# Kernel tuning notes

Measured on AMD Instinct MI355X. Metric: run time of the kernel, lower is better.

## Reference

```python
import jax, jax.numpy as jnp
import numpy as np

EPS = 1e-12  # tf.nn.l2_normalize epsilon


def _l2norm(x, axis):
    # tf.nn.l2_normalize: x / sqrt(max(sum(x^2), eps))
    return x * jax.lax.rsqrt(jnp.maximum(jnp.sum(x * x, axis=axis, keepdims=True), EPS))


def setup_inputs() -> dict:
    key = jax.random.key(0)
    k0, k1, k2, k3 = jax.random.split(key, 4)
    B, L, E, C, NG = 128, 1024, 300, 20, 55
    return {
        "x_emb": jax.random.normal(k0, (B, L, E), jnp.float32),
        "x_mask": jnp.ones((B, L), jnp.float32),            # mask_seq = tf.ones(...) in call()
        "W_class": jax.random.normal(k1, (B, C, E), jnp.float32),
        "conv_w": jax.random.normal(k2, (NG, C, C), jnp.float32) * 0.05,  # [width, in=C, out=C]
        "conv_b": jnp.zeros((C,), jnp.float32),
        "W_dis": jax.random.normal(k3, (C, E), jnp.float32) * 0.05,       # 20 per-class 0-layer discriminators
        "b_dis": jnp.zeros((C,), jnp.float32),
    }


def reference(x_emb, x_mask, W_class, conv_w, conv_b, W_dis, b_dis):
    # --- att_emb_ngram_encoder_cnn ---
    x0 = x_emb * x_mask[..., None]                       # b s e (masked word embeddings)
    xn = _l2norm(x0, 2)                                  # b s e
    wn = _l2norm(W_class, 2)                             # b c e (normalize over embed dim)
    G = jnp.einsum('bse,bce->bsc', xn, wn)               # cosine label-word attention, b s c
    # ngram conv smoothing over sequence, SAME padding, relu
    att = jax.lax.conv_general_dilated(
        G, conv_w, window_strides=(1,), padding='SAME',
        dimension_numbers=('NWC', 'WIO', 'NWC')) + conv_b  # b s c
    att = jax.nn.relu(att)
    # partial (masked) softmax over sequence dim
    ew = jnp.exp(att) * x_mask[..., None]                # b s c
    beta = ew / jnp.sum(ew, axis=1, keepdims=True)       # b s c
    # per-class attentive pooling of (unmasked) word embeddings: H_enc b e c
    H = jnp.einsum('bse,bsc->bec', x_emb, beta)
    # --- 20 per-class 0-layer discriminators (dropout is identity at inference) ---
    logits = jnp.einsum('bec,ce->bc', H, W_dis) + b_dis  # b c
    return logits
```

## Files before the change

### kernel.cpp

```cpp
#include <hip/hip_runtime.h>
#include <math.h>

#define B 128
#define L 1024
#define E 300
#define C 20

#define OFF_WNT 0
#define OFF_WDT 768000
#define OFF_SWC 774000
#define OFF_G   796400
#define OFF_D   3417840
#define OFF_S   6039280
#define OFF_T   6041840

__global__ __launch_bounds__(256) void prep_kernel(
    const float* __restrict__ Wc, const float* __restrict__ convw,
    const float* __restrict__ wdis,
    float* __restrict__ wnT, float* __restrict__ wdT,
    float* __restrict__ swc, float* __restrict__ ST)
{
  int t = threadIdx.x;
  int gid = blockIdx.x * 256 + t;

  if (gid < 2 * B * C) ST[gid] = 0.f;

  if (gid < 55 * C * C) {
    int w  = gid / (C * C);
    int r  = gid % (C * C);
    int ci = r / C, co = r % C;
    swc[(((size_t)ci * 4 + co / 5) * 14 + (w >> 2)) * 20 + (co % 5) * 4 + (w & 3)] = convw[gid];
  }
  if (gid < C * C) {
    int ci = gid / C, co = gid % C;
    swc[(((size_t)ci * 4 + co / 5) * 14 + 13) * 20 + (co % 5) * 4 + 3] = 0.f;
  }
  if (gid < 6000) {
    int og = gid / 1500, rem = gid % 1500;
    int kq = rem / 20, i = rem % 20;
    int co = og * 5 + i / 4, q = i & 3;
    wdT[gid] = wdis[(size_t)co * E + kq * 4 + q];
  }

  int row = blockIdx.x * 4 + (t >> 6);
  int ln  = t & 63;
  if (row < B * C) {
    int bb = row / C, c = row % C;
    const float* src = Wc + (size_t)row * E;
    float v[5];
    float ss = 0.f;
    #pragma unroll
    for (int k = 0; k < 5; ++k) {
      int e = ln + 64 * k;
      v[k] = (e < E) ? src[e] : 0.f;
      ss += v[k] * v[k];
    }
    #pragma unroll
    for (int off = 32; off; off >>= 1) ss += __shfl_xor(ss, off, 64);
    float r = rsqrtf(fmaxf(ss, 1e-12f));
    float* dst = wnT + ((size_t)bb * 4 + c / 5) * 1500;
    int cosub = (c % 5) * 4;
    #pragma unroll
    for (int k = 0; k < 5; ++k) {
      int e = ln + 64 * k;
      if (e < E) dst[(e >> 2) * 20 + cosub + (e & 3)] = v[k] * r;
    }
  }
}

__global__ __launch_bounds__(512, 4) void gemm_kernel(
    const float* __restrict__ x, const float* __restrict__ wnT,
    const float* __restrict__ wdT, float* __restrict__ Gt, float* __restrict__ Dt)
{
  __shared__ float xs[32 * 256];

  int t  = threadIdx.x;
  int ln = t & 63;
  int wid  = __builtin_amdgcn_readfirstlane(t >> 6);
  int og   = wid & 3;
  int role = wid >> 2;
  int b  = blockIdx.y;
  int s0 = blockIdx.x * 256;

  const float* wbase = (role == 0) ? (wnT + ((size_t)b * 4 + og) * 1500)
                                   : (wdT + (size_t)og * 1500);

  float acc[5][4];
  #pragma unroll
  for (int c = 0; c < 5; ++c)
    #pragma unroll
    for (int j = 0; j < 4; ++j) acc[c][j] = 0.f;
  float ssq[4] = {0.f, 0.f, 0.f, 0.f};

  for (int chunk = 0; chunk < 10; ++chunk) {
    int k0 = chunk * 32;
    int krem = E - k0; if (krem > 32) krem = 32;

    const float* xb = x + ((size_t)b * L + s0) * E + k0;
    #pragma unroll
    for (int it = 0; it < 4; ++it) {
      int idx = it * 512 + t;
      int row = idx >> 3, col = idx & 7;
      if (col * 4 < krem) {
        float4 f = *(const float4*)(xb + (size_t)row * E + col * 4);
        xs[(col * 4 + 0) * 256 + row] = f.x;
        xs[(col * 4 + 1) * 256 + row] = f.y;
        xs[(col * 4 + 2) * 256 + row] = f.z;
        xs[(col * 4 + 3) * 256 + row] = f.w;
      }
    }
    __syncthreads();

    int nq = krem >> 2;
    #pragma unroll
    for (int kq = 0; kq < 8; ++kq) {
      if (kq < nq) {
        const float* wp = wbase + (chunk * 8 + kq) * 20;
        float w[20];
        #pragma unroll
        for (int i = 0; i < 20; ++i) w[i] = wp[i];
        float4 xk[4];
        #pragma unroll
        for (int q = 0; q < 4; ++q)
          xk[q] = *(const float4*)&xs[(kq * 4 + q) * 256 + ln * 4];
        if (wid == 0) {
          #pragma unroll
          for (int q = 0; q < 4; ++q) {
            const float* xf = (const float*)&xk[q];
            #pragma unroll
            for (int j = 0; j < 4; ++j) ssq[j] = fmaf(xf[j], xf[j], ssq[j]);
          }
        }
        #pragma unroll
        for (int q = 0; q < 4; ++q) {
          const float* xf = (const float*)&xk[q];
          #pragma unroll
          for (int c = 0; c < 5; ++c) {
            float wv = w[c * 4 + q];
            #pragma unroll
            for (int j = 0; j < 4; ++j) acc[c][j] = fmaf(xf[j], wv, acc[c][j]);
          }
        }
      }
    }
    __syncthreads();
  }

  if (wid == 0) {
    #pragma unroll
    for (int j = 0; j < 4; ++j) xs[ln * 4 + j] = rsqrtf(fmaxf(ssq[j], 1e-12f));
  }
  __syncthreads();

  int s = s0 + ln * 4;
  if (role == 0) {
    float4 rv = *(const float4*)&xs[ln * 4];
    const float* rf = (const float*)&rv;
    #pragma unroll
    for (int c = 0; c < 5; ++c) {
      float4 o = { acc[c][0] * rf[0], acc[c][1] * rf[1],
                   acc[c][2] * rf[2], acc[c][3] * rf[3] };
      *(float4*)&Gt[((size_t)b * C + og * 5 + c) * L + s] = o;
    }
  } else {
    #pragma unroll
    for (int c = 0; c < 5; ++c) {
      float4 o = { acc[c][0], acc[c][1], acc[c][2], acc[c][3] };
      *(float4*)&Dt[((size_t)b * C + og * 5 + c) * L + s] = o;
    }
  }
}

#define GP 312
__global__ __launch_bounds__(512, 4) void conv_kernel(
    const float* __restrict__ Gt, const float* __restrict__ Dt,
    const float* __restrict__ swc, const float* __restrict__ convb,
    float* __restrict__ S, float* __restrict__ T)
{
  __shared__ float g_lds[C * GP];

  int t  = threadIdx.x;
  int ln = t & 63;
  int wid = __builtin_amdgcn_readfirstlane(t >> 6);
  int og  = wid & 3;
  int cih = wid >> 2;
  int b  = blockIdx.y;
  int s0 = blockIdx.x * 256;

  for (int c = 0; c < C; ++c)
    for (int h = t; h < GP; h += 512) {
      int s = s0 - 27 + h;
      g_lds[c * GP + h] = (s >= 0 && s < L) ? Gt[((size_t)b * C + c) * L + s] : 0.f;
    }
  __syncthreads();

  float acc[4][5];
  #pragma unroll
  for (int j = 0; j < 4; ++j)
    #pragma unroll
    for (int c = 0; c < 5; ++c) acc[j][c] = 0.f;

  for (int ci = cih * 10; ci < cih * 10 + 10; ++ci) {
    const float* gl = &g_lds[ci * GP + ln * 4];
    const float* wp = swc + ((size_t)ci * 4 + og) * 280;
    float4 g0 = *(const float4*)gl;
    #pragma unroll
    for (int wq = 0; wq < 14; ++wq) {
      float4 g1 = *(const float4*)(gl + wq * 4 + 4);
      float w[20];
      #pragma unroll
      for (int i = 0; i < 20; ++i) w[i] = wp[wq * 20 + i];
      float ga[7] = {g0.x, g0.y, g0.z, g0.w, g1.x, g1.y, g1.z};
      #pragma unroll
      for (int q = 0; q < 4; ++q) {
        #pragma unroll
        for (int j = 0; j < 4; ++j) {
          float gv = ga[q + j];
          #pragma unroll
          for (int c = 0; c < 5; ++c)
            acc[j][c] = fmaf(gv, w[c * 4 + q], acc[j][c]);
        }
      }
      g0 = g1;
    }
  }

  __syncthreads();
  float* scr = g_lds;
  int pr = (og * 64 + ln) * 21;
  if (cih == 1) {
    #pragma unroll
    for (int j = 0; j < 4; ++j)
      #pragma unroll
      for (int c = 0; c < 5; ++c) scr[pr + j * 5 + c] = acc[j][c];
  }
  __syncthreads();

  if (cih == 0) {
    #pragma unroll
    for (int j = 0; j < 4; ++j)
      #pragma unroll
      for (int c = 0; c < 5; ++c) acc[j][c] += scr[pr + j * 5 + c];

    float se[5], st_[5];
    int s = s0 + ln * 4;
    #pragma unroll
    for (int c = 0; c < 5; ++c) {
      float cb = convb[og * 5 + c];
      float4 d4 = *(const float4*)&Dt[((size_t)b * C + og * 5 + c) * L + s];
      const float* df = (const float*)&d4;
      float e0 = 0.f, e1 = 0.f;
      #pragma unroll
      for (int j = 0; j < 4; ++j) {
        float a = acc[j][c] + cb;
        float e = expf(fmaxf(a, 0.f));
        e0 += e;
        e1 += e * df[j];
      }
      se[c] = e0; st_[c] = e1;
    }
    #pragma unroll
    for (int c = 0; c < 5; ++c) {
      #pragma unroll
      for (int off = 32; off; off >>= 1) {
        se[c]  += __shfl_xor(se[c],  off, 64);
        st_[c] += __shfl_xor(st_[c], off, 64);
      }
    }
    if (ln == 0) {
      #pragma unroll
      for (int c = 0; c < 5; ++c) {
        atomicAdd(&S[b * C + og * 5 + c], se[c]);
        atomicAdd(&T[b * C + og * 5 + c], st_[c]);
      }
    }
  }
}

__global__ __launch_bounds__(256) void fin_kernel(
    const float* __restrict__ S, const float* __restrict__ T,
    const float* __restrict__ bdis, float* __restrict__ out)
{
  int i = blockIdx.x * 256 + threadIdx.x;
  if (i < B * C) out[i] = T[i] / S[i] + bdis[i % C];
}

extern "C" void kernel_launch(void* const* d_in, const int* in_sizes, int n_in,
                              void* d_out, int out_size, void* d_ws, size_t ws_size,
                              hipStream_t stream) {
  const float* x_emb = (const float*)d_in[0];
  const float* Wc    = (const float*)d_in[2];
  const float* convw = (const float*)d_in[3];
  const float* convb = (const float*)d_in[4];
  const float* wdis  = (const float*)d_in[5];
  const float* bdis  = (const float*)d_in[6];

  float* ws  = (float*)d_ws;
  float* wnT = ws + OFF_WNT;
  float* wdT = ws + OFF_WDT;
  float* swc = ws + OFF_SWC;
  float* Gt  = ws + OFF_G;
  float* Dt  = ws + OFF_D;
  float* S   = ws + OFF_S;
  float* T   = ws + OFF_T;
  float* out = (float*)d_out;

  prep_kernel<<<640, 256, 0, stream>>>(Wc, convw, wdis, wnT, wdT, swc, S);
  gemm_kernel<<<dim3(L / 256, B), 512, 0, stream>>>(x_emb, wnT, wdT, Gt, Dt);
  conv_kernel<<<dim3(L / 256, B), 512, 0, stream>>>(Gt, Dt, swc, convb, S, T);
  fin_kernel<<<10, 256, 0, stream>>>(S, T, bdis, out);
}
```

Measured before the change: 330.7 us.

## Retile projection GEMM with row-major padded LDS, register prefetch, wider output groups

The GEMM kernel is retiled to 128-row blocks of 256 threads. Each wave now computes 10 output columns for 2 rows instead of 5 columns for 4 rows, so the weight layouts in prep are regrouped into halves of 10 classes. x is stored row-major in LDS with a padded stride of 33, which replaces the transposed scalar stores with float4 stores. The next chunk is prefetched into registers while the current one is computed. Conv kernel launch bounds are raised to 6 blocks per CU, which trades register budget for occupancy and risks spills.

Result: slower. 427.9 us (+29.4%).

```diff
diff --git a/kernel.cpp b/kernel.cpp
--- a/kernel.cpp
+++ b/kernel.cpp
@@ -36,10 +36,10 @@
     swc[(((size_t)ci * 4 + co / 5) * 14 + 13) * 20 + (co % 5) * 4 + 3] = 0.f;
   }
   if (gid < 6000) {
-    int og = gid / 1500, rem = gid % 1500;
-    int kq = rem / 20, i = rem % 20;
-    int co = og * 5 + i / 4, q = i & 3;
-    wdT[gid] = wdis[(size_t)co * E + kq * 4 + q];
+    int h = gid / 3000, rem = gid % 3000;
+    int kq = rem / 40, i = rem % 40;
+    int o = i >> 2, q = i & 3;
+    wdT[gid] = wdis[(size_t)(h * 10 + o) * E + kq * 4 + q];
   }
 
   int row = blockIdx.x * 4 + (t >> 6);
@@ -58,87 +58,100 @@
     #pragma unroll
     for (int off = 32; off; off >>= 1) ss += __shfl_xor(ss, off, 64);
     float r = rsqrtf(fmaxf(ss, 1e-12f));
-    float* dst = wnT + ((size_t)bb * 4 + c / 5) * 1500;
-    int cosub = (c % 5) * 4;
+    float* dst = wnT + ((size_t)bb * 2 + c / 10) * 3000;
+    int cosub = (c % 10) * 4;
     #pragma unroll
     for (int k = 0; k < 5; ++k) {
       int e = ln + 64 * k;
-      if (e < E) dst[(e >> 2) * 20 + cosub + (e & 3)] = v[k] * r;
-    }
-  }
-}
-
-__global__ __launch_bounds__(512, 4) void gemm_kernel(
+      if (e < E) dst[(e >> 2) * 40 + cosub + (e & 3)] = v[k] * r;
+    }
+  }
+}
+
+#define KSTR 33
+__global__ __launch_bounds__(256, 4) void gemm_kernel(
     const float* __restrict__ x, const float* __restrict__ wnT,
     const float* __restrict__ wdT, float* __restrict__ Gt, float* __restrict__ Dt)
 {
-  __shared__ float xs[32 * 256];
+  __shared__ float xs[128 * KSTR];
+  __shared__ float rinvS[128];
 
   int t  = threadIdx.x;
   int ln = t & 63;
   int wid  = __builtin_amdgcn_readfirstlane(t >> 6);
-  int og   = wid & 3;
-  int role = wid >> 2;
+  int h    = wid & 1;
+  int role = wid >> 1;
   int b  = blockIdx.y;
-  int s0 = blockIdx.x * 256;
-
-  const float* wbase = (role == 0) ? (wnT + ((size_t)b * 4 + og) * 1500)
-                                   : (wdT + (size_t)og * 1500);
-
-  float acc[5][4];
+  int s0 = blockIdx.x * 128;
+
+  const float* wbase = (role == 0) ? (wnT + ((size_t)b * 2 + h) * 3000)
+                                   : (wdT + (size_t)h * 3000);
+  const float* xb = x + ((size_t)b * L + s0) * E;
+
+  float acc[10][2];
   #pragma unroll
-  for (int c = 0; c < 5; ++c)
-    #pragma unroll
-    for (int j = 0; j < 4; ++j) acc[c][j] = 0.f;
-  float ssq[4] = {0.f, 0.f, 0.f, 0.f};
+  for (int o = 0; o < 10; ++o) { acc[o][0] = 0.f; acc[o][1] = 0.f; }
+  float ssq0 = 0.f, ssq1 = 0.f;
+
+  float4 pf[4];
+  #pragma unroll
+  for (int it = 0; it < 4; ++it) {
+    int idx = it * 256 + t;
+    int row = idx >> 3, col = idx & 7;
+    pf[it] = *(const float4*)(xb + (size_t)row * E + col * 4);
+  }
 
   for (int chunk = 0; chunk < 10; ++chunk) {
     int k0 = chunk * 32;
     int krem = E - k0; if (krem > 32) krem = 32;
 
-    const float* xb = x + ((size_t)b * L + s0) * E + k0;
     #pragma unroll
     for (int it = 0; it < 4; ++it) {
-      int idx = it * 512 + t;
+      int idx = it * 256 + t;
       int row = idx >> 3, col = idx & 7;
-      if (col * 4 < krem) {
-        float4 f = *(const float4*)(xb + (size_t)row * E + col * 4);
-        xs[(col * 4 + 0) * 256 + row] = f.x;
-        xs[(col * 4 + 1) * 256 + row] = f.y;
-        xs[(col * 4 + 2) * 256 + row] = f.z;
-        xs[(col * 4 + 3) * 256 + row] = f.w;
-      }
+      if (col * 4 < krem) *(float4*)&xs[row * KSTR + col * 4] = pf[it];
     }
     __syncthreads();
 
+    if (chunk < 9) {
+      int nrem = E - (chunk + 1) * 32; if (nrem > 32) nrem = 32;
+      #pragma unroll
+      for (int it = 0; it < 4; ++it) {
+        int idx = it * 256 + t;
+        int row = idx >> 3, col = idx & 7;
+        if (col * 4 < nrem)
+          pf[it] = *(const float4*)(xb + (size_t)row * E + (chunk + 1) * 32 + col * 4);
+      }
+    }
+
     int nq = krem >> 2;
+    const float* r0p = &xs[(ln * 2) * KSTR];
+    const float* r1p = &xs[(ln * 2 + 1) * KSTR];
     #pragma unroll
     for (int kq = 0; kq < 8; ++kq) {
       if (kq < nq) {
-        const float* wp = wbase + (chunk * 8 + kq) * 20;
-        float w[20];
+        const float* wp = wbase + (chunk * 8 + kq) * 40;
+        float w[40];
         #pragma unroll
-        for (int i = 0; i < 20; ++i) w[i] = wp[i];
-        float4 xk[4];
-        #pragma unroll
-        for (int q = 0; q < 4; ++q)
-          xk[q] = *(const float4*)&xs[(kq * 4 + q) * 256 + ln * 4];
+        for (int i = 0; i < 40; ++i) w[i] = wp[i];
+        float4 x0 = *(const float4*)(r0p + kq * 4);
+        float4 x1 = *(const float4*)(r1p + kq * 4);
+        const float* f0 = (const float*)&x0;
+        const float* f1 = (const float*)&x1;
         if (wid == 0) {
           #pragma unroll
           for (int q = 0; q < 4; ++q) {
-            const float* xf = (const float*)&xk[q];
-            #pragma unroll
-            for (int j = 0; j < 4; ++j) ssq[j] = fmaf(xf[j], xf[j], ssq[j]);
+            ssq0 = fmaf(f0[q], f0[q], ssq0);
+            ssq1 = fmaf(f1[q], f1[q], ssq1);
           }
         }
         #pragma unroll
         for (int q = 0; q < 4; ++q) {
-          const float* xf = (const float*)&xk[q];
           #pragma unroll
-          for (int c = 0; c < 5; ++c) {
-            float wv = w[c * 4 + q];
-            #pragma unroll
-            for (int j = 0; j < 4; ++j) acc[c][j] = fmaf(xf[j], wv, acc[c][j]);
+          for (int o = 0; o < 10; ++o) {
+            float wv = w[o * 4 + q];
+            acc[o][0] = fmaf(f0[q], wv, acc[o][0]);
+            acc[o][1] = fmaf(f1[q], wv, acc[o][1]);
           }
         }
       }
@@ -147,32 +160,30 @@
   }
 
   if (wid == 0) {
-    #pragma unroll
-    for (int j = 0; j < 4; ++j) xs[ln * 4 + j] = rsqrtf(fmaxf(ssq[j], 1e-12f));
+    rinvS[ln * 2]     = rsqrtf(fmaxf(ssq0, 1e-12f));
+    rinvS[ln * 2 + 1] = rsqrtf(fmaxf(ssq1, 1e-12f));
   }
   __syncthreads();
 
-  int s = s0 + ln * 4;
+  int s = s0 + ln * 2;
   if (role == 0) {
-    float4 rv = *(const float4*)&xs[ln * 4];
-    const float* rf = (const float*)&rv;
-    #pragma unroll
-    for (int c = 0; c < 5; ++c) {
-      float4 o = { acc[c][0] * rf[0], acc[c][1] * rf[1],
-                   acc[c][2] * rf[2], acc[c][3] * rf[3] };
-      *(float4*)&Gt[((size_t)b * C + og * 5 + c) * L + s] = o;
+    float r0 = rinvS[ln * 2], r1 = rinvS[ln * 2 + 1];
+    #pragma unroll
+    for (int o = 0; o < 10; ++o) {
+      float2 ov = { acc[o][0] * r0, acc[o][1] * r1 };
+      *(float2*)&Gt[((size_t)b * C + h * 10 + o) * L + s] = ov;
     }
   } else {
     #pragma unroll
-    for (int c = 0; c < 5; ++c) {
-      float4 o = { acc[c][0], acc[c][1], acc[c][2], acc[c][3] };
-      *(float4*)&Dt[((size_t)b * C + og * 5 + c) * L + s] = o;
+    for (int o = 0; o < 10; ++o) {
+      float2 ov = { acc[o][0], acc[o][1] };
+      *(float2*)&Dt[((size_t)b * C + h * 10 + o) * L + s] = ov;
     }
   }
 }
 
 #define GP 312
-__global__ __launch_bounds__(512, 4) void conv_kernel(
+__global__ __launch_bounds__(512, 6) void conv_kernel(
     const float* __restrict__ Gt, const float* __restrict__ Dt,
     const float* __restrict__ swc, const float* __restrict__ convb,
     float* __restrict__ S, float* __restrict__ T)
@@ -306,7 +317,7 @@
   float* out = (float*)d_out;
 
   prep_kernel<<<640, 256, 0, stream>>>(Wc, convw, wdis, wnT, wdT, swc, S);
-  gemm_kernel<<<dim3(L / 256, B), 512, 0, stream>>>(x_emb, wnT, wdT, Gt, Dt);
+  gemm_kernel<<<dim3(L / 128, B), 256, 0, stream>>>(x_emb, wnT, wdT, Gt, Dt);
   conv_kernel<<<dim3(L / 256, B), 512, 0, stream>>>(Gt, Dt, swc, convb, S, T);
   fin_kernel<<<10, 256, 0, stream>>>(S, T, bdis, out);
 }
```
